# Kernel tuning notes

Measured on AMD Instinct MI355X. Metric: run time of the kernel, lower is better.

## Reference

```python
import jax, jax.numpy as jnp
import numpy as np

GAMMA = 1.0
ALPHA = 0.5
EMBED_DIM = 256
N = 8192
M = 8192


def setup_inputs() -> dict:
    key = jax.random.key(0)
    k1, k2, k3, k4 = jax.random.split(key, 4)
    a = jax.random.normal(k1, (N, EMBED_DIM), dtype=jnp.float32)
    b = jax.random.normal(k2, (M, EMBED_DIM), dtype=jnp.float32)
    # torch.nn.Linear default init: U(-1/sqrt(fan_in), 1/sqrt(fan_in))
    lim = 1.0 / np.sqrt(EMBED_DIM)
    Wq = jax.random.uniform(k3, (EMBED_DIM, EMBED_DIM), jnp.float32, -lim, lim)
    Wk = jax.random.uniform(k4, (EMBED_DIM, EMBED_DIM), jnp.float32, -lim, lim)
    return {"a": a, "b": b, "Wq": Wq, "Wk": Wk}


def reference(a, b, Wq, Wk):
    # Vectorized Gram matrix of HybridKernelMethod.forward over all (a_i, b_j) pairs.
    inv_sqrt_d = np.float32(1.0 / np.sqrt(EMBED_DIM))
    ab = a @ b.T                                           # [N, M] cross dot products
    # RBF part: ||a_i - b_j||^2 = ||a_i||^2 + ||b_j||^2 - 2 a_i.b_j
    sq = (jnp.sum(a * a, axis=-1)[:, None]
          + jnp.sum(b * b, axis=-1)[None, :] - 2.0 * ab)
    rbf_sim = jnp.exp(-GAMMA * sq)                         # [N, M]
    # Attention part: per pair, q k^T is a 1x1 matrix, so softmax == 1 exactly.
    q = a @ Wq.T                                           # [N, D]
    k = b @ Wk.T                                           # [M, D]
    s = (q @ k.T) * inv_sqrt_d                             # [N, M] scores
    scores = jax.nn.softmax(s[..., None], axis=-1)[..., 0]  # all-ones, faithful to 1x1 softmax
    attn_sim = scores * ab                                 # sum((scores @ v) * x) == scores * (a.b)
    return (1.0 - ALPHA) * rbf_sim + ALPHA * attn_sim      # [N, M] Gram matrix
```

## Files before the change

kernel.cpp:

```cpp
#include <hip/hip_runtime.h>
#include <stdint.h>

#define DIM 256
#define NR 8192
#define BM 128
#define BN 128
#define BK 32
#define GRID 4096

typedef __bf16 bf16x8 __attribute__((ext_vector_type(8)));
typedef float  f32x16 __attribute__((ext_vector_type(16)));
typedef float  f32x4  __attribute__((ext_vector_type(4)));

#define MEMFENCE asm volatile("" ::: "memory")
#define WAITV(N) asm volatile("s_waitcnt vmcnt(" #N ")" ::: "memory")
#define BAR __builtin_amdgcn_s_barrier()

__device__ __forceinline__ unsigned short f2bf_rne(float f) {
    unsigned int u = __float_as_uint(f);
    u += 0x7FFFu + ((u >> 16) & 1u);
    return (unsigned short)(u >> 16);
}

__global__ void prep_kernel(const float* __restrict__ a,
                            const float* __restrict__ b,
                            unsigned short* __restrict__ aB,
                            unsigned short* __restrict__ bB,
                            float* __restrict__ na,
                            float* __restrict__ nb) {
    const int w = threadIdx.x >> 6;
    const int l = threadIdx.x & 63;
    const int blk = blockIdx.x;
    const float* src; unsigned short* dst; float* nrm; int row;
    if (blk < 2048) { src = a; dst = aB; nrm = na; row = blk * 4 + w; }
    else            { src = b; dst = bB; nrm = nb; row = (blk - 2048) * 4 + w; }
    const float4 v = reinterpret_cast<const float4*>(src + (size_t)row * DIM)[l];
    float ss = v.x * v.x + v.y * v.y + v.z * v.z + v.w * v.w;
#pragma unroll
    for (int off = 32; off > 0; off >>= 1) ss += __shfl_down(ss, off);
    if (l == 0) nrm[row] = ss;
    ushort4 o = make_ushort4(f2bf_rne(v.x), f2bf_rne(v.y), f2bf_rne(v.z), f2bf_rne(v.w));
    reinterpret_cast<ushort4*>(dst + (size_t)row * DIM)[l] = o;
}

#define STAGE(kt_, buf_)                                                          \
    do {                                                                          \
        _Pragma("unroll")                                                         \
        for (int it_ = 0; it_ < 2; ++it_) {                                       \
            __builtin_amdgcn_global_load_lds(                                     \
                (const __attribute__((address_space(1))) void*)(aB +              \
                    (size_t)(row0 + w * 32 + it_ * 16 + rQ) * DIM + (kt_) * BK + cOf), \
                (__attribute__((address_space(3))) void*)&sA[buf_][(w * 2 + it_) * 512], \
                16, 0, 0);                                                        \
        }                                                                         \
        _Pragma("unroll")                                                         \
        for (int it_ = 0; it_ < 2; ++it_) {                                       \
            __builtin_amdgcn_global_load_lds(                                     \
                (const __attribute__((address_space(1))) void*)(bB +              \
                    (size_t)(col0 + w * 32 + it_ * 16 + rQ) * DIM + (kt_) * BK + cOf), \
                (__attribute__((address_space(3))) void*)&sB[buf_][(w * 2 + it_) * 512], \
                16, 0, 0);                                                        \
        }                                                                         \
    } while (0)

#define COMPUTE(buf_)                                                             \
    do {                                                                          \
        __builtin_amdgcn_s_setprio(1);                                            \
        _Pragma("unroll")                                                         \
        for (int ks_ = 0; ks_ < 2; ++ks_) {                                       \
            bf16x8 af[2], bfv[2];                                                 \
            _Pragma("unroll")                                                     \
            for (int mi_ = 0; mi_ < 2; ++mi_)                                     \
                af[mi_] = *(const bf16x8*)((const char*)&sA[buf_][0] +            \
                    baseA[mi_] + (((ks_ << 1) ^ XA[mi_]) << 4));                  \
            _Pragma("unroll")                                                     \
            for (int ni_ = 0; ni_ < 2; ++ni_)                                     \
                bfv[ni_] = *(const bf16x8*)((const char*)&sB[buf_][0] +           \
                    baseB[ni_] + (((ks_ << 1) ^ XB[ni_]) << 4));                  \
            _Pragma("unroll")                                                     \
            for (int mi_ = 0; mi_ < 2; ++mi_)                                     \
                _Pragma("unroll")                                                 \
                for (int ni_ = 0; ni_ < 2; ++ni_)                                 \
                    acc[mi_][ni_] = __builtin_amdgcn_mfma_f32_32x32x16_bf16(      \
                        af[mi_], bfv[ni_], acc[mi_][ni_], 0, 0, 0);               \
        }                                                                         \
        __builtin_amdgcn_s_setprio(0);                                            \
    } while (0)

__global__ __launch_bounds__(256, 4) void gemm_kernel(
        const unsigned short* __restrict__ aB,
        const unsigned short* __restrict__ bB,
        const float* __restrict__ na,
        const float* __restrict__ nb,
        float* __restrict__ out) {
    __shared__ unsigned short sA[2][4096];
    __shared__ unsigned short sB[2][4096];
    __shared__ float sNA[128];
    __shared__ float sNB[128];

    const int t = threadIdx.x;
    const int w = t >> 6, l = t & 63;
    const int wr = w >> 1, wc = w & 1;
    const int hi = l >> 5, lr = l & 31;

    const int bx = (int)blockIdx.x & 63;
    const int by = (int)blockIdx.x >> 6;
    const int col0 = bx * BN;
    const int row0 = by * BM;

    const int rQ = l >> 2;
    const int cOf = ((l & 3) ^ ((l >> 3) & 3)) * 8;

    int baseA[2], XA[2], baseB[2], XB[2];
#pragma unroll
    for (int mi = 0; mi < 2; ++mi) {
        const int r = wr * 64 + mi * 32 + lr;
        baseA[mi] = r * 64;
        XA[mi] = hi ^ ((r >> 1) & 3);
        const int rb = wc * 64 + mi * 32 + lr;
        baseB[mi] = rb * 64;
        XB[mi] = hi ^ ((rb >> 1) & 3);
    }

    f32x4 nIn;
    if (t < 32)      nIn = *(const f32x4*)&na[row0 + t * 4];
    else if (t < 64) nIn = *(const f32x4*)&nb[col0 + (t - 32) * 4];
    STAGE(0, 0);
    STAGE(1, 1);
    if (t < 32)      *(f32x4*)&sNA[t * 4] = nIn;
    else if (t < 64) *(f32x4*)&sNB[(t - 32) * 4] = nIn;
    asm volatile("s_waitcnt lgkmcnt(0)" ::: "memory");
    MEMFENCE;

    f32x16 acc[2][2];
#pragma unroll
    for (int mi = 0; mi < 2; ++mi)
#pragma unroll
        for (int ni = 0; ni < 2; ++ni) acc[mi][ni] = (f32x16)0.0f;

#pragma unroll
    for (int p = 0; p < 8; ++p) {
        if (p == 7) { WAITV(0); } else { WAITV(4); }
        BAR; MEMFENCE;
        COMPUTE(p & 1);
        MEMFENCE;
        if (p < 6) {
            BAR; MEMFENCE;
            STAGE(p + 2, p & 1);
            MEMFENCE;
        }
    }

    const int m4 = l & 3;
    const int colT = col0 + wc * 64 + (lr >> 2) * 4;
#pragma unroll
    for (int ni = 0; ni < 2; ++ni) {
        const float nbv = sNB[wc * 64 + ni * 32 + lr];
#pragma unroll
        for (int mi = 0; mi < 2; ++mi) {
#pragma unroll
            for (int p = 0; p < 4; ++p) {
                const f32x4 nv = *(const f32x4*)&sNA[wr * 64 + mi * 32 + 8 * p + 4 * hi];
                float av[4];
#pragma unroll
                for (int q = 0; q < 4; ++q) {
                    const float dot = acc[mi][ni][p * 4 + q];
                    const float sq = nv[q] + nbv - 2.0f * dot;
                    av[q] = 0.5f * __expf(-sq) + 0.5f * dot;
                }
                float tv;
                tv = __shfl_xor((m4 & 1) ? av[0] : av[1], 1);
                if (m4 & 1) av[0] = tv; else av[1] = tv;
                tv = __shfl_xor((m4 & 1) ? av[2] : av[3], 1);
                if (m4 & 1) av[2] = tv; else av[3] = tv;
                tv = __shfl_xor((m4 & 2) ? av[0] : av[2], 2);
                if (m4 & 2) av[0] = tv; else av[2] = tv;
                tv = __shfl_xor((m4 & 2) ? av[1] : av[3], 2);
                if (m4 & 2) av[1] = tv; else av[3] = tv;
                const int row = row0 + wr * 64 + mi * 32 + 8 * p + 4 * hi + m4;
                f32x4 st; st[0] = av[0]; st[1] = av[1]; st[2] = av[2]; st[3] = av[3];
                *(f32x4*)&out[(size_t)row * 8192 + colT + ni * 32] = st;
            }
        }
    }
}

__global__ void naive_kernel(const float* __restrict__ a,
                             const float* __restrict__ b,
                             float* __restrict__ out) {
    const size_t idx = (size_t)blockIdx.x * 256 + threadIdx.x;
    const int i = (int)(idx >> 13);
    const int j = (int)(idx & 8191);
    float dot = 0.f, naa = 0.f, nbb = 0.f;
    for (int k = 0; k < DIM; ++k) {
        const float x = a[(size_t)i * DIM + k];
        const float y = b[(size_t)j * DIM + k];
        dot += x * y; naa += x * x; nbb += y * y;
    }
    const float sq = naa + nbb - 2.0f * dot;
    out[idx] = 0.5f * __expf(-sq) + 0.5f * dot;
}

extern "C" void kernel_launch(void* const* d_in, const int* in_sizes, int n_in,
                              void* d_out, int out_size, void* d_ws, size_t ws_size,
                              hipStream_t stream) {
    const float* a = (const float*)d_in[0];
    const float* b = (const float*)d_in[1];
    float* out = (float*)d_out;

    const size_t bf_bytes = (size_t)NR * DIM * sizeof(unsigned short);
    const size_t nrm_bytes = (size_t)NR * sizeof(float);
    const size_t need = 2 * bf_bytes + 2 * nrm_bytes;

    if (ws_size >= need) {
        unsigned short* aBf = (unsigned short*)d_ws;
        unsigned short* bBf = (unsigned short*)((char*)d_ws + bf_bytes);
        float* na = (float*)((char*)d_ws + 2 * bf_bytes);
        float* nb = (float*)((char*)d_ws + 2 * bf_bytes + nrm_bytes);

        prep_kernel<<<4096, 256, 0, stream>>>(a, b, aBf, bBf, na, nb);
        gemm_kernel<<<GRID, 256, 0, stream>>>(aBf, bBf, na, nb, out);
    } else {
        naive_kernel<<<((size_t)NR * NR) / 256, 256, 0, stream>>>(a, b, out);
    }
}
```

Measured before the change: 87.17 us.

## Make each wave an independent 64x64 tile worker with barrier-free 4-slot pipeline

The block-cooperative 128x128 tile, double-buffered with block barriers, becomes per-wave independent 64x64 tiles. Each wave owns private LDS slots and runs a 4-deep global_load_lds ring over 16 K-chunks, and that ring carries across 8 consecutive column tiles. The grid shrinks to 512 persistent-style blocks. The aim is to drop s_barrier stalls and to overlap the next tile's loads with the epilogue, at the cost of no A/B sharing between waves and lower MFMA-to-load reuse per tile.

```diff
diff --git a/kernel.cpp b/kernel.cpp
--- a/kernel.cpp
+++ b/kernel.cpp
@@ -3,18 +3,15 @@
 
 #define DIM 256
 #define NR 8192
-#define BM 128
-#define BN 128
-#define BK 32
-#define GRID 4096
 
 typedef __bf16 bf16x8 __attribute__((ext_vector_type(8)));
 typedef float  f32x16 __attribute__((ext_vector_type(16)));
 typedef float  f32x4  __attribute__((ext_vector_type(4)));
 
-#define MEMFENCE asm volatile("" ::: "memory")
 #define WAITV(N) asm volatile("s_waitcnt vmcnt(" #N ")" ::: "memory")
-#define BAR __builtin_amdgcn_s_barrier()
+#define GLDS(src, dst, sz) __builtin_amdgcn_global_load_lds( \
+    (const __attribute__((address_space(1))) void*)(src),    \
+    (__attribute__((address_space(3))) void*)(dst), sz, 0, 0)
 
 __device__ __forceinline__ unsigned short f2bf_rne(float f) {
     unsigned int u = __float_as_uint(f);
@@ -43,143 +40,126 @@
     reinterpret_cast<ushort4*>(dst + (size_t)row * DIM)[l] = o;
 }
 
-#define STAGE(kt_, buf_)                                                          \
-    do {                                                                          \
-        _Pragma("unroll")                                                         \
-        for (int it_ = 0; it_ < 2; ++it_) {                                       \
-            __builtin_amdgcn_global_load_lds(                                     \
-                (const __attribute__((address_space(1))) void*)(aB +              \
-                    (size_t)(row0 + w * 32 + it_ * 16 + rQ) * DIM + (kt_) * BK + cOf), \
-                (__attribute__((address_space(3))) void*)&sA[buf_][(w * 2 + it_) * 512], \
-                16, 0, 0);                                                        \
-        }                                                                         \
-        _Pragma("unroll")                                                         \
-        for (int it_ = 0; it_ < 2; ++it_) {                                       \
-            __builtin_amdgcn_global_load_lds(                                     \
-                (const __attribute__((address_space(1))) void*)(bB +              \
-                    (size_t)(col0 + w * 32 + it_ * 16 + rQ) * DIM + (kt_) * BK + cOf), \
-                (__attribute__((address_space(3))) void*)&sB[buf_][(w * 2 + it_) * 512], \
-                16, 0, 0);                                                        \
-        }                                                                         \
-    } while (0)
-
-#define COMPUTE(buf_)                                                             \
-    do {                                                                          \
-        __builtin_amdgcn_s_setprio(1);                                            \
-        _Pragma("unroll")                                                         \
-        for (int ks_ = 0; ks_ < 2; ++ks_) {                                       \
-            bf16x8 af[2], bfv[2];                                                 \
-            _Pragma("unroll")                                                     \
-            for (int mi_ = 0; mi_ < 2; ++mi_)                                     \
-                af[mi_] = *(const bf16x8*)((const char*)&sA[buf_][0] +            \
-                    baseA[mi_] + (((ks_ << 1) ^ XA[mi_]) << 4));                  \
-            _Pragma("unroll")                                                     \
-            for (int ni_ = 0; ni_ < 2; ++ni_)                                     \
-                bfv[ni_] = *(const bf16x8*)((const char*)&sB[buf_][0] +           \
-                    baseB[ni_] + (((ks_ << 1) ^ XB[ni_]) << 4));                  \
-            _Pragma("unroll")                                                     \
-            for (int mi_ = 0; mi_ < 2; ++mi_)                                     \
-                _Pragma("unroll")                                                 \
-                for (int ni_ = 0; ni_ < 2; ++ni_)                                 \
-                    acc[mi_][ni_] = __builtin_amdgcn_mfma_f32_32x32x16_bf16(      \
-                        af[mi_], bfv[ni_], acc[mi_][ni_], 0, 0, 0);               \
-        }                                                                         \
-        __builtin_amdgcn_s_setprio(0);                                            \
-    } while (0)
-
-__global__ __launch_bounds__(256, 4) void gemm_kernel(
+__global__ __launch_bounds__(256) void gemm_kernel(
         const unsigned short* __restrict__ aB,
         const unsigned short* __restrict__ bB,
         const float* __restrict__ na,
         const float* __restrict__ nb,
         float* __restrict__ out) {
-    __shared__ unsigned short sA[2][4096];
-    __shared__ unsigned short sB[2][4096];
-    __shared__ float sNA[128];
-    __shared__ float sNB[128];
+    __shared__ unsigned short sA[4][4][1024];
+    __shared__ unsigned short sB[4][4][1024];
+    __shared__ float sN[4][64];
 
     const int t = threadIdx.x;
     const int w = t >> 6, l = t & 63;
-    const int wr = w >> 1, wc = w & 1;
-    const int hi = l >> 5, lr = l & 31;
-
-    const int bx = (int)blockIdx.x & 63;
-    const int by = (int)blockIdx.x >> 6;
-    const int col0 = bx * BN;
-    const int row0 = by * BM;
-
-    const int rQ = l >> 2;
-    const int cOf = ((l & 3) ^ ((l >> 3) & 3)) * 8;
-
-    int baseA[2], XA[2], baseB[2], XB[2];
+    const int hi = l >> 5, lr = l & 31, m4 = l & 3;
+
+    const int gw = (int)blockIdx.x * 4 + w;
+    const int row0 = (gw & 127) * 64;
+    const int col00 = (gw >> 7) * 64;
+
+    int rSt[2], gSt[2];
+#pragma unroll
+    for (int i = 0; i < 2; ++i) {
+        const int G = i * 64 + l;
+        const int q = G >> 5, m = (G >> 1) & 15;
+        rSt[i] = q * 16 + m;
+        gSt[i] = ((G & 1) ^ (q & 1) ^ ((m >> 2) & 1) ^ ((m >> 3) & 1)) * 8;
+    }
+    int offA[2];
 #pragma unroll
     for (int mi = 0; mi < 2; ++mi) {
-        const int r = wr * 64 + mi * 32 + lr;
-        baseA[mi] = r * 64;
-        XA[mi] = hi ^ ((r >> 1) & 3);
-        const int rb = wc * 64 + mi * 32 + lr;
-        baseB[mi] = rb * 64;
-        XB[mi] = hi ^ ((rb >> 1) & 3);
-    }
-
-    f32x4 nIn;
-    if (t < 32)      nIn = *(const f32x4*)&na[row0 + t * 4];
-    else if (t < 64) nIn = *(const f32x4*)&nb[col0 + (t - 32) * 4];
-    STAGE(0, 0);
-    STAGE(1, 1);
-    if (t < 32)      *(f32x4*)&sNA[t * 4] = nIn;
-    else if (t < 64) *(f32x4*)&sNB[(t - 32) * 4] = nIn;
-    asm volatile("s_waitcnt lgkmcnt(0)" ::: "memory");
-    MEMFENCE;
-
-    f32x16 acc[2][2];
-#pragma unroll
-    for (int mi = 0; mi < 2; ++mi)
-#pragma unroll
-        for (int ni = 0; ni < 2; ++ni) acc[mi][ni] = (f32x16)0.0f;
-
-#pragma unroll
-    for (int p = 0; p < 8; ++p) {
-        if (p == 7) { WAITV(0); } else { WAITV(4); }
-        BAR; MEMFENCE;
-        COMPUTE(p & 1);
-        MEMFENCE;
-        if (p < 6) {
-            BAR; MEMFENCE;
-            STAGE(p + 2, p & 1);
-            MEMFENCE;
+        const int r = mi * 32 + lr;
+        const int q = r >> 4, m = r & 15;
+        const int p = hi ^ (q & 1) ^ ((m >> 2) & 1) ^ ((m >> 3) & 1);
+        offA[mi] = (q * 32 + m * 2 + p) * 16;
+    }
+
+    GLDS(na + row0 + l, &sN[w][0], 4);
+#pragma unroll
+    for (int c = 0; c < 3; ++c) {
+#pragma unroll
+        for (int i = 0; i < 2; ++i)
+            GLDS(aB + (size_t)(row0 + rSt[i]) * DIM + c * 16 + gSt[i],
+                 &sA[w][c][i * 512], 16);
+#pragma unroll
+        for (int i = 0; i < 2; ++i)
+            GLDS(bB + (size_t)(col00 + rSt[i]) * DIM + c * 16 + gSt[i],
+                 &sB[w][c][i * 512], 16);
+    }
+
+    for (int ti = 0; ti < 8; ++ti) {
+        const int col0 = col00 + ti * 1024;
+        const float nbv0 = nb[col0 + lr];
+        const float nbv1 = nb[col0 + 32 + lr];
+
+        f32x16 acc[2][2];
+#pragma unroll
+        for (int mi = 0; mi < 2; ++mi)
+#pragma unroll
+            for (int ni = 0; ni < 2; ++ni) acc[mi][ni] = (f32x16)0.0f;
+
+#pragma unroll
+        for (int c = 0; c < 16; ++c) {
+            if (c <= 1)       { WAITV(10); }
+            else if (c == 14) { if (ti == 7) { WAITV(4); } else { WAITV(8); } }
+            else if (c == 15) { if (ti == 7) { WAITV(0); } else { WAITV(8); } }
+            else              { WAITV(8); }
+
+            if (c < 13 || ti < 7) {
+                const int sc = (c + 3) & 15;
+                const int slot = (c + 3) & 3;
+                const int colS = (c >= 13) ? col0 + 1024 : col0;
+#pragma unroll
+                for (int i = 0; i < 2; ++i)
+                    GLDS(aB + (size_t)(row0 + rSt[i]) * DIM + sc * 16 + gSt[i],
+                         &sA[w][slot][i * 512], 16);
+#pragma unroll
+                for (int i = 0; i < 2; ++i)
+                    GLDS(bB + (size_t)(colS + rSt[i]) * DIM + sc * 16 + gSt[i],
+                         &sB[w][slot][i * 512], 16);
+            }
+
+            const int sl = c & 3;
+            const bf16x8 a0 = *(const bf16x8*)((const char*)&sA[w][sl][0] + offA[0]);
+            const bf16x8 a1 = *(const bf16x8*)((const char*)&sA[w][sl][0] + offA[1]);
+            const bf16x8 b0 = *(const bf16x8*)((const char*)&sB[w][sl][0] + offA[0]);
+            const bf16x8 b1 = *(const bf16x8*)((const char*)&sB[w][sl][0] + offA[1]);
+            acc[0][0] = __builtin_amdgcn_mfma_f32_32x32x16_bf16(a0, b0, acc[0][0], 0, 0, 0);
+            acc[0][1] = __builtin_amdgcn_mfma_f32_32x32x16_bf16(a0, b1, acc[0][1], 0, 0, 0);
+            acc[1][0] = __builtin_amdgcn_mfma_f32_32x32x16_bf16(a1, b0, acc[1][0], 0, 0, 0);
+            acc[1][1] = __builtin_amdgcn_mfma_f32_32x32x16_bf16(a1, b1, acc[1][1], 0, 0, 0);
         }
-    }
-
-    const int m4 = l & 3;
-    const int colT = col0 + wc * 64 + (lr >> 2) * 4;
-#pragma unroll
-    for (int ni = 0; ni < 2; ++ni) {
-        const float nbv = sNB[wc * 64 + ni * 32 + lr];
-#pragma unroll
-        for (int mi = 0; mi < 2; ++mi) {
-#pragma unroll
-            for (int p = 0; p < 4; ++p) {
-                const f32x4 nv = *(const f32x4*)&sNA[wr * 64 + mi * 32 + 8 * p + 4 * hi];
-                float av[4];
-#pragma unroll
-                for (int q = 0; q < 4; ++q) {
-                    const float dot = acc[mi][ni][p * 4 + q];
-                    const float sq = nv[q] + nbv - 2.0f * dot;
-                    av[q] = 0.5f * __expf(-sq) + 0.5f * dot;
+
+        const int colT = col0 + (lr >> 2) * 4;
+#pragma unroll
+        for (int ni = 0; ni < 2; ++ni) {
+            const float nbv = ni ? nbv1 : nbv0;
+#pragma unroll
+            for (int mi = 0; mi < 2; ++mi) {
+#pragma unroll
+                for (int p = 0; p < 4; ++p) {
+                    const f32x4 nv = *(const f32x4*)&sN[w][mi * 32 + 8 * p + 4 * hi];
+                    float av[4];
+#pragma unroll
+                    for (int q = 0; q < 4; ++q) {
+                        const float dot = acc[mi][ni][p * 4 + q];
+                        const float sq = nv[q] + nbv - 2.0f * dot;
+                        av[q] = 0.5f * __expf(-sq) + 0.5f * dot;
+                    }
+                    float tv;
+                    tv = __shfl_xor((m4 & 1) ? av[0] : av[1], 1);
+                    if (m4 & 1) av[0] = tv; else av[1] = tv;
+                    tv = __shfl_xor((m4 & 1) ? av[2] : av[3], 1);
+                    if (m4 & 1) av[2] = tv; else av[3] = tv;
+                    tv = __shfl_xor((m4 & 2) ? av[0] : av[2], 2);
+                    if (m4 & 2) av[0] = tv; else av[2] = tv;
+                    tv = __shfl_xor((m4 & 2) ? av[1] : av[3], 2);
+                    if (m4 & 2) av[1] = tv; else av[3] = tv;
+                    const int row = row0 + mi * 32 + 8 * p + 4 * hi + m4;
+                    f32x4 st; st[0] = av[0]; st[1] = av[1]; st[2] = av[2]; st[3] = av[3];
+                    *(f32x4*)&out[(size_t)row * 8192 + colT + ni * 32] = st;
                 }
-                float tv;
-                tv = __shfl_xor((m4 & 1) ? av[0] : av[1], 1);
-                if (m4 & 1) av[0] = tv; else av[1] = tv;
-                tv = __shfl_xor((m4 & 1) ? av[2] : av[3], 1);
-                if (m4 & 1) av[2] = tv; else av[3] = tv;
-                tv = __shfl_xor((m4 & 2) ? av[0] : av[2], 2);
-                if (m4 & 2) av[0] = tv; else av[2] = tv;
-                tv = __shfl_xor((m4 & 2) ? av[1] : av[3], 2);
-                if (m4 & 2) av[1] = tv; else av[3] = tv;
-                const int row = row0 + wr * 64 + mi * 32 + 8 * p + 4 * hi + m4;
-                f32x4 st; st[0] = av[0]; st[1] = av[1]; st[2] = av[2]; st[3] = av[3];
-                *(f32x4*)&out[(size_t)row * 8192 + colT + ni * 32] = st;
             }
         }
     }
@@ -219,7 +199,7 @@
         float* nb = (float*)((char*)d_ws + 2 * bf_bytes + nrm_bytes);
 
         prep_kernel<<<4096, 256, 0, stream>>>(a, b, aBf, bBf, na, nb);
-        gemm_kernel<<<GRID, 256, 0, stream>>>(aBf, bBf, na, nb, out);
+        gemm_kernel<<<512, 256, 0, stream>>>(aBf, bBf, na, nb, out);
     } else {
         naive_kernel<<<((size_t)NR * NR) / 256, 256, 0, stream>>>(a, b, out);
     }
```

New measurement: 133.7 us. 1.53x slower.
